# Kernel optimization log

Hardware: AMD Instinct MI355X
Metric: run time of the kernel (lower is better)

The kernel has to match this reference:

```python
import jax, jax.numpy as jnp
import numpy as np

N_EMBD = 384
HEAD_SIZE = 64
BLOCK_SIZE = 64
SCALE = HEAD_SIZE * N_EMBD ** (-0.5)  # non-standard scale from source: k.shape[-1] * C**-0.5


def setup_inputs() -> dict:
    key = jax.random.key(0)
    kx, kk, kq, kv = jax.random.split(key, 4)
    B, T = 2048, BLOCK_SIZE
    x = jax.random.normal(kx, (B, T, N_EMBD), dtype=jnp.float32)
    # torch Linear(n_embd, head_size, bias=False): weight shape [head_size, n_embd], y = x @ W.T
    s = N_EMBD ** -0.5
    Wk = jax.random.uniform(kk, (HEAD_SIZE, N_EMBD), jnp.float32, -s, s)
    Wq = jax.random.uniform(kq, (HEAD_SIZE, N_EMBD), jnp.float32, -s, s)
    Wv = jax.random.uniform(kv, (HEAD_SIZE, N_EMBD), jnp.float32, -s, s)
    return {"x": x, "Wk": Wk, "Wq": Wq, "Wv": Wv}


def reference(x, Wk, Wq, Wv) -> jnp.ndarray:
    B, T, C = x.shape
    k = jnp.einsum("btc,hc->bth", x, Wk)  # [B,T,H]
    q = jnp.einsum("btc,hc->bth", x, Wq)
    v = jnp.einsum("btc,hc->bth", x, Wv)
    wei = jnp.einsum("bth,bsh->bts", q, k) * SCALE  # [B,T,T]
    causal = jnp.tril(jnp.ones((T, T), dtype=bool))
    wei = jnp.where(causal, wei, -jnp.inf)
    wei = jax.nn.softmax(wei, axis=-1)
    out = jnp.einsum("bts,bsh->bth", wei, v)  # [B,T,H]
    return out
```

## Files before the change

### kernel.cpp

```cpp
#include <hip/hip_runtime.h>

typedef _Float16 f16;
typedef _Float16 f16x8 __attribute__((ext_vector_type(8)));
typedef _Float16 f16x4 __attribute__((ext_vector_type(4)));
typedef float    f32x4 __attribute__((ext_vector_type(4)));

#define MFMA16(a, b, c) __builtin_amdgcn_mfma_f32_16x16x32_f16((a), (b), (c), 0, 0, 0)

constexpr int T = 64;
constexpr int C = 384;
constexpr int H = 64;
constexpr float SCALE = 3.26598632371090f;

__device__ __forceinline__ void load_lds16(const float* g, float* l) {
  __builtin_amdgcn_global_load_lds(
      (const __attribute__((address_space(1))) void*)g,
      (__attribute__((address_space(3))) void*)l, 16, 0, 0);
}

__global__ void pack_w(const float* __restrict__ Wk, const float* __restrict__ Wq,
                       const float* __restrict__ Wv, f16* __restrict__ Wp) {
  int tid = blockIdx.x * blockDim.x + threadIdx.x;
  if (tid >= 3 * 12 * 4 * 64) return;
  int lane = tid & 63;
  int tile = tid >> 6;
  int ht = tile & 3;
  int kt = (tile >> 2) % 12;
  int wi = tile / 48;
  const float* W = (wi == 0) ? Wk : ((wi == 1) ? Wq : Wv);
  int h = 16 * ht + (lane & 15);
  int c = 32 * kt + 8 * (lane >> 4);
  const float* src = W + h * C + c;
  f16x8 v;
#pragma unroll
  for (int j = 0; j < 8; ++j) v[j] = (f16)src[j];
  *(f16x8*)(Wp + (size_t)tile * 512 + lane * 8) = v;
}

__global__ __launch_bounds__(256, 3) void head_fused(
    const float* __restrict__ x, const f16* __restrict__ Wp,
    float* __restrict__ out) {
  __shared__ float xc[2][2048];
  __shared__ f16 qp_lds[64][72];
  __shared__ f16 k_lds[64][72];
  __shared__ f16 vT_lds[64][72];

  const int b = blockIdx.x;
  const int tid = threadIdx.x;
  const int w = tid >> 6;
  const int lane = tid & 63;
  const int l15 = lane & 15;
  const int g = lane >> 4;
  const int t_ = 16 * w + l15;

  const f32x4 vzero = {0.0f, 0.0f, 0.0f, 0.0f};
  f32x4 acc[3][4];
#pragma unroll
  for (int c = 0; c < 3; ++c)
#pragma unroll
    for (int tt = 0; tt < 4; ++tt) acc[c][tt] = vzero;

  const f16* wp_base[3];
  bool isV[3];
#pragma unroll
  for (int c = 0; c < 3; ++c) {
    int combo = 3 * w + c;
    int m = combo >> 2;
    int ht = combo & 3;
    wp_base[c] = Wp + (size_t)(m * 48 + ht) * 512 + lane * 8;
    isV[c] = (combo >= 8);
  }

  const float* xbase = x + (size_t)b * T * C;
  const float* gsrc = xbase + (size_t)(16 * w + l15) * C + g * 8;

  load_lds16(gsrc + 0 * 32 + 0, &xc[0][(2 * w + 0) * 256]);
  load_lds16(gsrc + 0 * 32 + 4, &xc[0][(2 * w + 1) * 256]);
  f16x8 wpc[3], wpn[3];
#pragma unroll
  for (int c = 0; c < 3; ++c) wpc[c] = *(const f16x8*)(wp_base[c]);

#pragma unroll 2
  for (int kt = 0; kt < 12; ++kt) {
    const int cur = kt & 1;
    if (kt + 1 < 12) {
      load_lds16(gsrc + (kt + 1) * 32 + 0, &xc[cur ^ 1][(2 * w + 0) * 256]);
      load_lds16(gsrc + (kt + 1) * 32 + 4, &xc[cur ^ 1][(2 * w + 1) * 256]);
#pragma unroll
      for (int c = 0; c < 3; ++c)
        wpn[c] = *(const f16x8*)(wp_base[c] + (size_t)(kt + 1) * 2048);
    }
    __builtin_amdgcn_s_waitcnt(0x0f70);
    __syncthreads();

    f16x8 xf[4];
#pragma unroll
    for (int tt = 0; tt < 4; ++tt) {
      f32x4 A0 = *(const f32x4*)&xc[cur][(2 * tt + 0) * 256 + lane * 4];
      f32x4 A1 = *(const f32x4*)&xc[cur][(2 * tt + 1) * 256 + lane * 4];
#pragma unroll
      for (int j = 0; j < 4; ++j) { xf[tt][j] = (f16)A0[j]; xf[tt][4 + j] = (f16)A1[j]; }
    }
#pragma unroll
    for (int c = 0; c < 3; ++c) {
      f16x8 wf = wpc[c];
      if (!isV[c]) {
#pragma unroll
        for (int tt = 0; tt < 4; ++tt) acc[c][tt] = MFMA16(wf, xf[tt], acc[c][tt]);
      } else {
#pragma unroll
        for (int tt = 0; tt < 4; ++tt) acc[c][tt] = MFMA16(xf[tt], wf, acc[c][tt]);
      }
      wpc[c] = wpn[c];
    }
    __syncthreads();
  }

#pragma unroll
  for (int c = 0; c < 3; ++c) {
    int combo = 3 * w + c;
    int m = combo >> 2;
    int ht = combo & 3;
#pragma unroll
    for (int tt = 0; tt < 4; ++tt) {
      f16x4 pd;
#pragma unroll
      for (int r = 0; r < 4; ++r) pd[r] = (f16)acc[c][tt][r];
      if (m == 0) {
        *(f16x4*)&k_lds[16 * tt + l15][16 * ht + 4 * g] = pd;
      } else if (m == 1) {
        *(f16x4*)&qp_lds[16 * tt + l15][16 * ht + 4 * g] = pd;
      } else {
        *(f16x4*)&vT_lds[16 * ht + l15][16 * tt + 4 * g] = pd;
      }
    }
  }
  __syncthreads();

  f32x4 accs[4];
#pragma unroll
  for (int i = 0; i < 4; ++i) accs[i] = vzero;
#pragma unroll
  for (int kt = 0; kt < 2; ++kt) {
    f16x8 qf = *(const f16x8*)&qp_lds[t_][32 * kt + 8 * g];
#pragma unroll
    for (int mt = 0; mt < 4; ++mt) {
      f16x8 kf = *(const f16x8*)&k_lds[16 * mt + l15][32 * kt + 8 * g];
      accs[mt] = MFMA16(kf, qf, accs[mt]);
    }
  }

  float e[16];
  float mx = -__builtin_inff();
#pragma unroll
  for (int mt = 0; mt < 4; ++mt) {
#pragma unroll
    for (int r = 0; r < 4; ++r) {
      int s = 16 * mt + 4 * g + r;
      float lv = accs[mt][r] * SCALE;
      lv = (s <= t_) ? lv : -__builtin_inff();
      e[mt * 4 + r] = lv;
      mx = fmaxf(mx, lv);
    }
  }
  mx = fmaxf(mx, __shfl_xor(mx, 16));
  mx = fmaxf(mx, __shfl_xor(mx, 32));
  float sm = 0.0f;
#pragma unroll
  for (int i = 0; i < 16; ++i) { e[i] = __expf(e[i] - mx); sm += e[i]; }
  sm += __shfl_xor(sm, 16);
  sm += __shfl_xor(sm, 32);
  const float inv = 1.0f / sm;
#pragma unroll
  for (int mt = 0; mt < 4; ++mt) {
    f16x4 pp;
#pragma unroll
    for (int r = 0; r < 4; ++r) pp[r] = (f16)(e[mt * 4 + r] * inv);
    *(f16x4*)&qp_lds[t_][16 * mt + 4 * g] = pp;
  }

  f32x4 acco[4];
#pragma unroll
  for (int i = 0; i < 4; ++i) acco[i] = vzero;
#pragma unroll
  for (int kt = 0; kt < 2; ++kt) {
    f16x8 pf = *(const f16x8*)&qp_lds[t_][32 * kt + 8 * g];
#pragma unroll
    for (int mt = 0; mt < 4; ++mt) {
      f16x8 vf = *(const f16x8*)&vT_lds[16 * mt + l15][32 * kt + 8 * g];
      acco[mt] = MFMA16(vf, pf, acco[mt]);
    }
  }

  float* orow = out + ((size_t)b * T + t_) * H;
#pragma unroll
  for (int mt = 0; mt < 4; ++mt) {
    *(f32x4*)(orow + 16 * mt + 4 * g) = acco[mt];
  }
}

extern "C" void kernel_launch(void* const* d_in, const int* in_sizes, int n_in,
                              void* d_out, int out_size, void* d_ws, size_t ws_size,
                              hipStream_t stream) {
  const float* x  = (const float*)d_in[0];
  const float* Wk = (const float*)d_in[1];
  const float* Wq = (const float*)d_in[2];
  const float* Wv = (const float*)d_in[3];
  float* out = (float*)d_out;
  f16* Wp = (f16*)d_ws;

  pack_w<<<36, 256, 0, stream>>>(Wk, Wq, Wv, Wp);
  head_fused<<<2048, 256, 0, stream>>>(x, Wp, out);
}
```

Measured before the change: 304.3 us.

## Give each wave its own token rows and load x directly into registers

The projection work is repartitioned so each wave owns 16 token rows and computes all 12 K/Q/V head tiles for them. Previously each wave owned 3 head tiles across all 64 tokens. x is now read straight from global memory into registers with a register double buffer, which removes the LDS x staging buffer and the two block barriers per k-step. The packed weights are reordered so all 12 tiles for one k-step are contiguous. In exchange, each wave now loads 12 weight fragments per step instead of 3, and register pressure rises.

```diff
diff --git a/kernel.cpp b/kernel.cpp
--- a/kernel.cpp
+++ b/kernel.cpp
@@ -11,12 +11,6 @@
 constexpr int C = 384;
 constexpr int H = 64;
 constexpr float SCALE = 3.26598632371090f;
-
-__device__ __forceinline__ void load_lds16(const float* g, float* l) {
-  __builtin_amdgcn_global_load_lds(
-      (const __attribute__((address_space(1))) void*)g,
-      (__attribute__((address_space(3))) void*)l, 16, 0, 0);
-}
 
 __global__ void pack_w(const float* __restrict__ Wk, const float* __restrict__ Wq,
                        const float* __restrict__ Wv, f16* __restrict__ Wp) {
@@ -34,13 +28,13 @@
   f16x8 v;
 #pragma unroll
   for (int j = 0; j < 8; ++j) v[j] = (f16)src[j];
-  *(f16x8*)(Wp + (size_t)tile * 512 + lane * 8) = v;
+  int tile2 = kt * 12 + wi * 4 + ht;
+  *(f16x8*)(Wp + (size_t)tile2 * 512 + lane * 8) = v;
 }
 
 __global__ __launch_bounds__(256, 3) void head_fused(
     const float* __restrict__ x, const f16* __restrict__ Wp,
     float* __restrict__ out) {
-  __shared__ float xc[2][2048];
   __shared__ f16 qp_lds[64][72];
   __shared__ f16 k_lds[64][72];
   __shared__ f16 vT_lds[64][72];
@@ -54,85 +48,51 @@
   const int t_ = 16 * w + l15;
 
   const f32x4 vzero = {0.0f, 0.0f, 0.0f, 0.0f};
-  f32x4 acc[3][4];
+  f32x4 acc[12];
 #pragma unroll
-  for (int c = 0; c < 3; ++c)
-#pragma unroll
-    for (int tt = 0; tt < 4; ++tt) acc[c][tt] = vzero;
+  for (int cb = 0; cb < 12; ++cb) acc[cb] = vzero;
 
-  const f16* wp_base[3];
-  bool isV[3];
-#pragma unroll
-  for (int c = 0; c < 3; ++c) {
-    int combo = 3 * w + c;
-    int m = combo >> 2;
-    int ht = combo & 3;
-    wp_base[c] = Wp + (size_t)(m * 48 + ht) * 512 + lane * 8;
-    isV[c] = (combo >= 8);
-  }
+  const float* gsrc = x + (size_t)b * T * C + (size_t)(16 * w + l15) * C + 8 * g;
+  const f16* wsrc = Wp + lane * 8;
 
-  const float* xbase = x + (size_t)b * T * C;
-  const float* gsrc = xbase + (size_t)(16 * w + l15) * C + g * 8;
-
-  load_lds16(gsrc + 0 * 32 + 0, &xc[0][(2 * w + 0) * 256]);
-  load_lds16(gsrc + 0 * 32 + 4, &xc[0][(2 * w + 1) * 256]);
-  f16x8 wpc[3], wpn[3];
-#pragma unroll
-  for (int c = 0; c < 3; ++c) wpc[c] = *(const f16x8*)(wp_base[c]);
-
+  f32x4 A0 = *(const f32x4*)(gsrc + 0);
+  f32x4 A1 = *(const f32x4*)(gsrc + 4);
 #pragma unroll 2
   for (int kt = 0; kt < 12; ++kt) {
-    const int cur = kt & 1;
+    f32x4 B0, B1;
     if (kt + 1 < 12) {
-      load_lds16(gsrc + (kt + 1) * 32 + 0, &xc[cur ^ 1][(2 * w + 0) * 256]);
-      load_lds16(gsrc + (kt + 1) * 32 + 4, &xc[cur ^ 1][(2 * w + 1) * 256]);
+      B0 = *(const f32x4*)(gsrc + (kt + 1) * 32 + 0);
+      B1 = *(const f32x4*)(gsrc + (kt + 1) * 32 + 4);
+    }
+    f16x8 wf[12];
 #pragma unroll
-      for (int c = 0; c < 3; ++c)
-        wpn[c] = *(const f16x8*)(wp_base[c] + (size_t)(kt + 1) * 2048);
-    }
-    __builtin_amdgcn_s_waitcnt(0x0f70);
-    __syncthreads();
-
-    f16x8 xf[4];
+    for (int cb = 0; cb < 12; ++cb)
+      wf[cb] = *(const f16x8*)(wsrc + ((size_t)kt * 12 + cb) * 512);
+    f16x8 xf;
 #pragma unroll
-    for (int tt = 0; tt < 4; ++tt) {
-      f32x4 A0 = *(const f32x4*)&xc[cur][(2 * tt + 0) * 256 + lane * 4];
-      f32x4 A1 = *(const f32x4*)&xc[cur][(2 * tt + 1) * 256 + lane * 4];
+    for (int j = 0; j < 4; ++j) { xf[j] = (f16)A0[j]; xf[4 + j] = (f16)A1[j]; }
 #pragma unroll
-      for (int j = 0; j < 4; ++j) { xf[tt][j] = (f16)A0[j]; xf[tt][4 + j] = (f16)A1[j]; }
-    }
+    for (int cb = 0; cb < 8; ++cb)
+      acc[cb] = MFMA16(wf[cb], xf, acc[cb]);
 #pragma unroll
-    for (int c = 0; c < 3; ++c) {
-      f16x8 wf = wpc[c];
-      if (!isV[c]) {
-#pragma unroll
-        for (int tt = 0; tt < 4; ++tt) acc[c][tt] = MFMA16(wf, xf[tt], acc[c][tt]);
-      } else {
-#pragma unroll
-        for (int tt = 0; tt < 4; ++tt) acc[c][tt] = MFMA16(xf[tt], wf, acc[c][tt]);
-      }
-      wpc[c] = wpn[c];
-    }
-    __syncthreads();
+    for (int cb = 8; cb < 12; ++cb)
+      acc[cb] = MFMA16(xf, wf[cb], acc[cb]);
+    A0 = B0; A1 = B1;
   }
 
 #pragma unroll
-  for (int c = 0; c < 3; ++c) {
-    int combo = 3 * w + c;
-    int m = combo >> 2;
-    int ht = combo & 3;
+  for (int cb = 0; cb < 12; ++cb) {
+    int m = cb >> 2;
+    int ht = cb & 3;
+    f16x4 pd;
 #pragma unroll
-    for (int tt = 0; tt < 4; ++tt) {
-      f16x4 pd;
-#pragma unroll
-      for (int r = 0; r < 4; ++r) pd[r] = (f16)acc[c][tt][r];
-      if (m == 0) {
-        *(f16x4*)&k_lds[16 * tt + l15][16 * ht + 4 * g] = pd;
-      } else if (m == 1) {
-        *(f16x4*)&qp_lds[16 * tt + l15][16 * ht + 4 * g] = pd;
-      } else {
-        *(f16x4*)&vT_lds[16 * ht + l15][16 * tt + 4 * g] = pd;
-      }
+    for (int r = 0; r < 4; ++r) pd[r] = (f16)acc[cb][r];
+    if (m == 0) {
+      *(f16x4*)&k_lds[16 * w + l15][16 * ht + 4 * g] = pd;
+    } else if (m == 1) {
+      *(f16x4*)&qp_lds[16 * w + l15][16 * ht + 4 * g] = pd;
+    } else {
+      *(f16x4*)&vT_lds[16 * ht + l15][16 * w + 4 * g] = pd;
     }
   }
   __syncthreads();
```

Result: slower. 330.0 us (+8.4%).

## Split fused head kernel into projection and attention kernels via global fp16 K/Q/V

Applied to the files above, without the earlier changes.

Splits the single fused kernel into a projection kernel that writes fp16 K, Q and transposed V to workspace and a separate attention kernel that reloads them. Each kernel now uses less LDS, so the launch bounds allow more resident blocks per CU. It also repacks the weights so all three matrices for a k-step sit together, fully unrolls the k-loop, and waits with explicit vmcnt(0) plus a barrier. The price is an extra kernel launch and a global round trip of about 50 MB of fp16 intermediates.

```diff
diff --git a/kernel.cpp b/kernel.cpp
--- a/kernel.cpp
+++ b/kernel.cpp
@@ -34,13 +34,116 @@
   f16x8 v;
 #pragma unroll
   for (int j = 0; j < 8; ++j) v[j] = (f16)src[j];
-  *(f16x8*)(Wp + (size_t)tile * 512 + lane * 8) = v;
-}
-
-__global__ __launch_bounds__(256, 3) void head_fused(
+  int tile2 = kt * 12 + wi * 4 + ht;
+  *(f16x8*)(Wp + (size_t)tile2 * 512 + lane * 8) = v;
+}
+
+__global__ __launch_bounds__(256, 4) void proj_kqv(
     const float* __restrict__ x, const f16* __restrict__ Wp,
-    float* __restrict__ out) {
+    f16* __restrict__ kg, f16* __restrict__ qg, f16* __restrict__ vtg) {
   __shared__ float xc[2][2048];
+
+  const int b = blockIdx.x;
+  const int tid = threadIdx.x;
+  const int w = tid >> 6;
+  const int lane = tid & 63;
+  const int l15 = lane & 15;
+  const int g = lane >> 4;
+
+  const f32x4 vzero = {0.0f, 0.0f, 0.0f, 0.0f};
+  f32x4 acc[3][4];
+#pragma unroll
+  for (int c = 0; c < 3; ++c)
+#pragma unroll
+    for (int tt = 0; tt < 4; ++tt) acc[c][tt] = vzero;
+
+  const f16* wp_base[3];
+  bool isV[3];
+#pragma unroll
+  for (int c = 0; c < 3; ++c) {
+    int combo = 3 * w + c;
+    wp_base[c] = Wp + (size_t)combo * 512 + lane * 8;
+    isV[c] = (combo >= 8);
+  }
+
+  const float* xbase = x + (size_t)b * T * C;
+  const float* gsrc = xbase + (size_t)(16 * w + l15) * C + g * 8;
+
+  load_lds16(gsrc + 0, &xc[0][(2 * w + 0) * 256]);
+  load_lds16(gsrc + 4, &xc[0][(2 * w + 1) * 256]);
+  f16x8 wpc[3], wpn[3];
+#pragma unroll
+  for (int c = 0; c < 3; ++c) wpc[c] = *(const f16x8*)(wp_base[c]);
+  asm volatile("s_waitcnt vmcnt(0)" ::: "memory");
+  __builtin_amdgcn_s_barrier();
+
+#pragma unroll
+  for (int kt = 0; kt < 12; ++kt) {
+    const int cur = kt & 1;
+    if (kt + 1 < 12) {
+      load_lds16(gsrc + (kt + 1) * 32 + 0, &xc[cur ^ 1][(2 * w + 0) * 256]);
+      load_lds16(gsrc + (kt + 1) * 32 + 4, &xc[cur ^ 1][(2 * w + 1) * 256]);
+#pragma unroll
+      for (int c = 0; c < 3; ++c)
+        wpn[c] = *(const f16x8*)(wp_base[c] + (size_t)(kt + 1) * 6144);
+    }
+
+    f16x8 xf[4];
+#pragma unroll
+    for (int tt = 0; tt < 4; ++tt) {
+      f32x4 A0 = *(const f32x4*)&xc[cur][(2 * tt + 0) * 256 + lane * 4];
+      f32x4 A1 = *(const f32x4*)&xc[cur][(2 * tt + 1) * 256 + lane * 4];
+#pragma unroll
+      for (int j = 0; j < 4; ++j) { xf[tt][j] = (f16)A0[j]; xf[tt][4 + j] = (f16)A1[j]; }
+    }
+#pragma unroll
+    for (int c = 0; c < 3; ++c) {
+      f16x8 wf = wpc[c];
+      if (!isV[c]) {
+#pragma unroll
+        for (int tt = 0; tt < 4; ++tt) acc[c][tt] = MFMA16(wf, xf[tt], acc[c][tt]);
+      } else {
+#pragma unroll
+        for (int tt = 0; tt < 4; ++tt) acc[c][tt] = MFMA16(xf[tt], wf, acc[c][tt]);
+      }
+      wpc[c] = wpn[c];
+    }
+    asm volatile("s_waitcnt vmcnt(0)" ::: "memory");
+    __builtin_amdgcn_s_barrier();
+  }
+
+  f16* vt_lds = (f16*)&xc[0][0];
+#pragma unroll
+  for (int c = 0; c < 3; ++c) {
+    int combo = 3 * w + c;
+    int m = combo >> 2;
+    int ht = combo & 3;
+#pragma unroll
+    for (int tt = 0; tt < 4; ++tt) {
+      f16x4 pd;
+#pragma unroll
+      for (int r = 0; r < 4; ++r) pd[r] = (f16)acc[c][tt][r];
+      if (m == 0) {
+        *(f16x4*)(kg + ((size_t)b * 64 + 16 * tt + l15) * 64 + 16 * ht + 4 * g) = pd;
+      } else if (m == 1) {
+        *(f16x4*)(qg + ((size_t)b * 64 + 16 * tt + l15) * 64 + 16 * ht + 4 * g) = pd;
+      } else {
+        *(f16x4*)&vt_lds[(16 * ht + l15) * 68 + 16 * tt + 4 * g] = pd;
+      }
+    }
+  }
+  __syncthreads();
+#pragma unroll
+  for (int r = 0; r < 2; ++r) {
+    int idx = tid + r * 256;
+    f16x8 vv = *(const f16x8*)&vt_lds[(idx >> 3) * 68 + (idx & 7) * 8];
+    *(f16x8*)(vtg + (size_t)b * 4096 + idx * 8) = vv;
+  }
+}
+
+__global__ __launch_bounds__(256, 5) void attn64(
+    const f16* __restrict__ kg, const f16* __restrict__ qg,
+    const f16* __restrict__ vtg, float* __restrict__ out) {
   __shared__ f16 qp_lds[64][72];
   __shared__ f16 k_lds[64][72];
   __shared__ f16 vT_lds[64][72];
@@ -53,89 +156,23 @@
   const int g = lane >> 4;
   const int t_ = 16 * w + l15;
 
+  const size_t tb = (size_t)b * 4096;
+  const int i0 = tid, i1 = tid + 256;
+  f16x8 ka = *(const f16x8*)(kg + tb + (size_t)i0 * 8);
+  f16x8 kb = *(const f16x8*)(kg + tb + (size_t)i1 * 8);
+  f16x8 qa = *(const f16x8*)(qg + tb + (size_t)i0 * 8);
+  f16x8 qb = *(const f16x8*)(qg + tb + (size_t)i1 * 8);
+  f16x8 va = *(const f16x8*)(vtg + tb + (size_t)i0 * 8);
+  f16x8 vb = *(const f16x8*)(vtg + tb + (size_t)i1 * 8);
+  *(f16x8*)&k_lds[i0 >> 3][(i0 & 7) * 8] = ka;
+  *(f16x8*)&k_lds[i1 >> 3][(i1 & 7) * 8] = kb;
+  *(f16x8*)&qp_lds[i0 >> 3][(i0 & 7) * 8] = qa;
+  *(f16x8*)&qp_lds[i1 >> 3][(i1 & 7) * 8] = qb;
+  *(f16x8*)&vT_lds[i0 >> 3][(i0 & 7) * 8] = va;
+  *(f16x8*)&vT_lds[i1 >> 3][(i1 & 7) * 8] = vb;
+  __syncthreads();
+
   const f32x4 vzero = {0.0f, 0.0f, 0.0f, 0.0f};
-  f32x4 acc[3][4];
-#pragma unroll
-  for (int c = 0; c < 3; ++c)
-#pragma unroll
-    for (int tt = 0; tt < 4; ++tt) acc[c][tt] = vzero;
-
-  const f16* wp_base[3];
-  bool isV[3];
-#pragma unroll
-  for (int c = 0; c < 3; ++c) {
-    int combo = 3 * w + c;
-    int m = combo >> 2;
-    int ht = combo & 3;
-    wp_base[c] = Wp + (size_t)(m * 48 + ht) * 512 + lane * 8;
-    isV[c] = (combo >= 8);
-  }
-
-  const float* xbase = x + (size_t)b * T * C;
-  const float* gsrc = xbase + (size_t)(16 * w + l15) * C + g * 8;
-
-  load_lds16(gsrc + 0 * 32 + 0, &xc[0][(2 * w + 0) * 256]);
-  load_lds16(gsrc + 0 * 32 + 4, &xc[0][(2 * w + 1) * 256]);
-  f16x8 wpc[3], wpn[3];
-#pragma unroll
-  for (int c = 0; c < 3; ++c) wpc[c] = *(const f16x8*)(wp_base[c]);
-
-#pragma unroll 2
-  for (int kt = 0; kt < 12; ++kt) {
-    const int cur = kt & 1;
-    if (kt + 1 < 12) {
-      load_lds16(gsrc + (kt + 1) * 32 + 0, &xc[cur ^ 1][(2 * w + 0) * 256]);
-      load_lds16(gsrc + (kt + 1) * 32 + 4, &xc[cur ^ 1][(2 * w + 1) * 256]);
-#pragma unroll
-      for (int c = 0; c < 3; ++c)
-        wpn[c] = *(const f16x8*)(wp_base[c] + (size_t)(kt + 1) * 2048);
-    }
-    __builtin_amdgcn_s_waitcnt(0x0f70);
-    __syncthreads();
-
-    f16x8 xf[4];
-#pragma unroll
-    for (int tt = 0; tt < 4; ++tt) {
-      f32x4 A0 = *(const f32x4*)&xc[cur][(2 * tt + 0) * 256 + lane * 4];
-      f32x4 A1 = *(const f32x4*)&xc[cur][(2 * tt + 1) * 256 + lane * 4];
-#pragma unroll
-      for (int j = 0; j < 4; ++j) { xf[tt][j] = (f16)A0[j]; xf[tt][4 + j] = (f16)A1[j]; }
-    }
-#pragma unroll
-    for (int c = 0; c < 3; ++c) {
-      f16x8 wf = wpc[c];
-      if (!isV[c]) {
-#pragma unroll
-        for (int tt = 0; tt < 4; ++tt) acc[c][tt] = MFMA16(wf, xf[tt], acc[c][tt]);
-      } else {
-#pragma unroll
-        for (int tt = 0; tt < 4; ++tt) acc[c][tt] = MFMA16(xf[tt], wf, acc[c][tt]);
-      }
-      wpc[c] = wpn[c];
-    }
-    __syncthreads();
-  }
-
-#pragma unroll
-  for (int c = 0; c < 3; ++c) {
-    int combo = 3 * w + c;
-    int m = combo >> 2;
-    int ht = combo & 3;
-#pragma unroll
-    for (int tt = 0; tt < 4; ++tt) {
-      f16x4 pd;
-#pragma unroll
-      for (int r = 0; r < 4; ++r) pd[r] = (f16)acc[c][tt][r];
-      if (m == 0) {
-        *(f16x4*)&k_lds[16 * tt + l15][16 * ht + 4 * g] = pd;
-      } else if (m == 1) {
-        *(f16x4*)&qp_lds[16 * tt + l15][16 * ht + 4 * g] = pd;
-      } else {
-        *(f16x4*)&vT_lds[16 * ht + l15][16 * tt + 4 * g] = pd;
-      }
-    }
-  }
-  __syncthreads();
 
   f32x4 accs[4];
 #pragma unroll
@@ -207,8 +244,13 @@
   const float* Wq = (const float*)d_in[2];
   const float* Wv = (const float*)d_in[3];
   float* out = (float*)d_out;
-  f16* Wp = (f16*)d_ws;
+
+  f16* Wp  = (f16*)d_ws;
+  f16* kg  = (f16*)((char*)d_ws + (1 << 18));
+  f16* qg  = kg + (size_t)2048 * 64 * 64;
+  f16* vtg = qg + (size_t)2048 * 64 * 64;
 
   pack_w<<<36, 256, 0, stream>>>(Wk, Wq, Wv, Wp);
-  head_fused<<<2048, 256, 0, stream>>>(x, Wp, out);
-}
+  proj_kqv<<<2048, 256, 0, stream>>>(x, Wp, kg, qg, vtg);
+  attn64<<<2048, 256, 0, stream>>>(kg, qg, vtg, out);
+}
```

After: 354.4 us. 1.16x slower.
